# Kernel optimization log

Hardware: AMD Instinct MI355X
Metric: run time of the kernel (lower is better)

Reference implementation:

```python
import jax, jax.numpy as jnp
import numpy as np

NUM_HEADS = 12
HEAD_DIM = 64  # d_out // num_heads = 768 // 12


def setup_inputs() -> dict:
    key = jax.random.key(0)
    k1, k2 = jax.random.split(key)
    x = jax.random.normal(k1, (2, 2048, 768), dtype=jnp.float32)
    # torch Linear weight: [d_out, d_in], y = x @ W.T
    Wq = jax.random.normal(k2, (768, 768), dtype=jnp.float32) * 0.02
    return {"x": x, "Wq": Wq}


def reference(x, Wq):
    b, n, d_in = x.shape
    H, hd = NUM_HEADS, HEAD_DIM
    d_out = H * hd
    # NOTE: the original module uses Wq for queries, keys AND values.
    qkv = x @ Wq.T                                   # [b, n, d_out]
    h = qkv.reshape(b, n, H, hd).transpose(0, 2, 1, 3)  # [b, H, n, hd]
    scores = jnp.einsum('bhqd,bhkd->bhqk', h, h)      # [b, H, n, n]
    causal = jnp.triu(jnp.ones((n, n), dtype=bool), k=1)
    scores = jnp.where(causal, -jnp.inf, scores)
    attn = jax.nn.softmax(scores / jnp.sqrt(jnp.float32(hd)), axis=-1)
    ctx = jnp.einsum('bhqk,bhkd->bhqd', attn, h)      # [b, H, n, hd]
    # faithful to source: transpose(-2,-1) -> [b, H, hd, n], then view(b, n, d_out)
    ctx = ctx.transpose(0, 1, 3, 2)
    return ctx.reshape(b, n, d_out)
```

## Files before the change

kernel.cpp:

```cpp
#include <hip/hip_runtime.h>
#include <math.h>

typedef __attribute__((ext_vector_type(8))) short  short8;
typedef __attribute__((ext_vector_type(4))) float  floatx4;

#define MFMA16(a, b, c) __builtin_amdgcn_mfma_f32_16x16x32_bf16(a, b, c, 0, 0, 0)

constexpr int NSEQ = 2048;
constexpr int DIN  = 768;
constexpr int NH   = 12;
constexpr size_t NX = (size_t)2 * NSEQ * DIN;
constexpr size_t NW = (size_t)DIN * DIN;
constexpr float QSCALE = 0.18033688011112042f;

__device__ __forceinline__ ushort f2bf(float f) {
    unsigned u = __float_as_uint(f);
    u += 0x7FFF + ((u >> 16) & 1);
    return (ushort)(u >> 16);
}
__device__ __forceinline__ float bf2f(ushort u) {
    return __uint_as_float(((unsigned)u) << 16);
}
__device__ __forceinline__ unsigned cvt_pk_bf16(float lo, float hi) {
    unsigned r;
    asm("v_cvt_pk_bf16_f32 %0, %1, %2" : "=v"(r) : "v"(lo), "v"(hi));
    return r;
}

__global__ __launch_bounds__(256)
void cvt_bf16(const float* __restrict__ x, const float* __restrict__ Wq,
              ushort* __restrict__ dst)
{
    size_t i = ((size_t)blockIdx.x * 256 + threadIdx.x) * 8;
    const float* s = (i < NX) ? (x + i) : (Wq + (i - NX));
    float4 f0 = ((const float4*)s)[0];
    float4 f1 = ((const float4*)s)[1];
    short8 o;
    o[0] = (short)f2bf(f0.x); o[1] = (short)f2bf(f0.y);
    o[2] = (short)f2bf(f0.z); o[3] = (short)f2bf(f0.w);
    o[4] = (short)f2bf(f1.x); o[5] = (short)f2bf(f1.y);
    o[6] = (short)f2bf(f1.z); o[7] = (short)f2bf(f1.w);
    *(short8*)(dst + i) = o;
}

__global__ __launch_bounds__(256, 3)
void qkv_mfma(const ushort* __restrict__ xb, const ushort* __restrict__ wb,
              ushort* __restrict__ h)
{
    __shared__ ushort As[64 * 72];
    __shared__ ushort Bs[64 * 72];

    const int tid  = threadIdx.x;
    const int w    = tid >> 6;
    const int lane = tid & 63;
    const int m    = lane & 15;
    const int quad = lane >> 4;
    const int r0   = blockIdx.x * 64;
    const int c0   = blockIdx.y * 64;
    const int mrow0 = (w & 1) * 32;
    const int ncol0 = (w >> 1) * 32;

    floatx4 C[2][2] = {};
    short8 ar[2], br[2];

    #pragma unroll
    for (int i = 0; i < 2; ++i) {
        int id = tid + i * 256;
        ar[i] = *(const short8*)(xb + (size_t)(r0 + (id >> 3)) * DIN + (id & 7) * 8);
        br[i] = *(const short8*)(wb + (size_t)(c0 + (id >> 3)) * DIN + (id & 7) * 8);
    }

    for (int kk = 0; kk < 12; ++kk) {
        __syncthreads();
        #pragma unroll
        for (int i = 0; i < 2; ++i) {
            int id = tid + i * 256;
            *(short8*)&As[(id >> 3) * 72 + (id & 7) * 8] = ar[i];
            *(short8*)&Bs[(id >> 3) * 72 + (id & 7) * 8] = br[i];
        }
        if (kk < 11) {
            const int k0 = (kk + 1) * 64;
            #pragma unroll
            for (int i = 0; i < 2; ++i) {
                int id = tid + i * 256;
                ar[i] = *(const short8*)(xb + (size_t)(r0 + (id >> 3)) * DIN + k0 + (id & 7) * 8);
                br[i] = *(const short8*)(wb + (size_t)(c0 + (id >> 3)) * DIN + k0 + (id & 7) * 8);
            }
        }
        __syncthreads();

        #pragma unroll
        for (int kt2 = 0; kt2 < 2; ++kt2) {
            short8 a0 = *(const short8*)&As[(mrow0 + m)      * 72 + kt2 * 32 + quad * 8];
            short8 a1 = *(const short8*)&As[(mrow0 + 16 + m) * 72 + kt2 * 32 + quad * 8];
            short8 b0 = *(const short8*)&Bs[(ncol0 + m)      * 72 + kt2 * 32 + quad * 8];
            short8 b1 = *(const short8*)&Bs[(ncol0 + 16 + m) * 72 + kt2 * 32 + quad * 8];
            C[0][0] = MFMA16(a0, b0, C[0][0]);
            C[0][1] = MFMA16(a0, b1, C[0][1]);
            C[1][0] = MFMA16(a1, b0, C[1][0]);
            C[1][1] = MFMA16(a1, b1, C[1][1]);
        }
    }

    #pragma unroll
    for (int mt = 0; mt < 2; ++mt)
        #pragma unroll
        for (int nt = 0; nt < 2; ++nt) {
            int cg = c0 + ncol0 + nt * 16 + m;
            int head = cg >> 6, d = cg & 63;
            #pragma unroll
            for (int r = 0; r < 4; ++r) {
                int rg = r0 + mrow0 + mt * 16 + quad * 4 + r;
                int b = rg >> 11, q = rg & 2047;
                h[((size_t)(b * NH + head) * NSEQ + q) * 64 + d] = f2bf(C[mt][nt][r]);
            }
        }
}

__global__ __launch_bounds__(128, 3)
void attn_mfma(const ushort* __restrict__ h, float* __restrict__ out)
{
    __shared__ ushort Ks[64 * 72];
    __shared__ ushort Vt[64 * 72];
    __shared__ ushort Ps[2 * 16 * 72];

    const int tid  = threadIdx.x;
    const int w    = tid >> 6;
    const int lane = tid & 63;
    const int m    = lane & 15;
    const int quad = lane >> 4;

    const int xi = blockIdx.x;
    const int bh = blockIdx.y;
    const int t  = bh >> 2;
    const int qt = (t & 1) ? xi : (63 - xi);
    const int q0 = qt * 32;
    const int wq = q0 + w * 16;
    const int nkt = (qt >> 1) + 1;
    const ushort* __restrict__ Hh = h + (size_t)bh * NSEQ * 64;

    short8 qa[2];
    #pragma unroll
    for (int kt2 = 0; kt2 < 2; ++kt2) {
        short8 raw = *(const short8*)(Hh + (size_t)(wq + m) * 64 + kt2 * 32 + quad * 8);
        #pragma unroll
        for (int j = 0; j < 8; ++j)
            qa[kt2][j] = (short)f2bf(bf2f((ushort)raw[j]) * QSCALE);
    }

    floatx4 O[4] = {};
    float lacc = 0.0f;
    ushort* Psw = Ps + w * 16 * 72;

    const int kr2  = (tid & 31) * 2;
    const int part = tid >> 5;
    const int db   = part * 16;

    short8 pre[4];
    {
        const ushort* src = Hh + (size_t)kr2 * 64 + db;
        pre[0] = *(const short8*)src;
        pre[1] = *(const short8*)(src + 8);
        pre[2] = *(const short8*)(src + 64);
        pre[3] = *(const short8*)(src + 72);
    }

    for (int kt = 0; kt < nkt; ++kt) {
        __syncthreads();
        *(short8*)&Ks[kr2       * 72 + db]     = pre[0];
        *(short8*)&Ks[kr2       * 72 + db + 8] = pre[1];
        *(short8*)&Ks[(kr2 + 1) * 72 + db]     = pre[2];
        *(short8*)&Ks[(kr2 + 1) * 72 + db + 8] = pre[3];
        union { short8 v; ushort u[8]; } a0, a1, b0, b1;
        a0.v = pre[0]; a1.v = pre[1]; b0.v = pre[2]; b1.v = pre[3];
        #pragma unroll
        for (int i = 0; i < 8; ++i) {
            *(unsigned*)&Vt[(db + i)     * 72 + kr2] = (unsigned)a0.u[i] | ((unsigned)b0.u[i] << 16);
            *(unsigned*)&Vt[(db + 8 + i) * 72 + kr2] = (unsigned)a1.u[i] | ((unsigned)b1.u[i] << 16);
        }
        if (kt + 1 < nkt) {
            const ushort* src = Hh + (size_t)((kt + 1) * 64 + kr2) * 64 + db;
            pre[0] = *(const short8*)src;
            pre[1] = *(const short8*)(src + 8);
            pre[2] = *(const short8*)(src + 64);
            pre[3] = *(const short8*)(src + 72);
        }
        __syncthreads();

        floatx4 S[4] = {};
        #pragma unroll
        for (int kt2 = 0; kt2 < 2; ++kt2)
            #pragma unroll
            for (int mt = 0; mt < 4; ++mt) {
                short8 ka = *(const short8*)&Ks[(mt * 16 + m) * 72 + kt2 * 32 + quad * 8];
                S[mt] = MFMA16(ka, qa[kt2], S[mt]);
            }

        const int lim = wq + m - kt * 64;
        if (kt == nkt - 1) {
            #pragma unroll
            for (int mt = 0; mt < 4; ++mt) {
                float p0 = (mt * 16 + quad * 4 + 0 <= lim) ? exp2f(S[mt][0]) : 0.0f;
                float p1 = (mt * 16 + quad * 4 + 1 <= lim) ? exp2f(S[mt][1]) : 0.0f;
                float p2 = (mt * 16 + quad * 4 + 2 <= lim) ? exp2f(S[mt][2]) : 0.0f;
                float p3 = (mt * 16 + quad * 4 + 3 <= lim) ? exp2f(S[mt][3]) : 0.0f;
                lacc += (p0 + p1) + (p2 + p3);
                uint2 pw;
                pw.x = cvt_pk_bf16(p0, p1);
                pw.y = cvt_pk_bf16(p2, p3);
                *(uint2*)&Psw[m * 72 + mt * 16 + quad * 4] = pw;
            }
        } else {
            #pragma unroll
            for (int mt = 0; mt < 4; ++mt) {
                float p0 = exp2f(S[mt][0]);
                float p1 = exp2f(S[mt][1]);
                float p2 = exp2f(S[mt][2]);
                float p3 = exp2f(S[mt][3]);
                lacc += (p0 + p1) + (p2 + p3);
                uint2 pw;
                pw.x = cvt_pk_bf16(p0, p1);
                pw.y = cvt_pk_bf16(p2, p3);
                *(uint2*)&Psw[m * 72 + mt * 16 + quad * 4] = pw;
            }
        }

        #pragma unroll
        for (int kt2 = 0; kt2 < 2; ++kt2) {
            short8 pb = *(const short8*)&Psw[m * 72 + kt2 * 32 + quad * 8];
            #pragma unroll
            for (int mt = 0; mt < 4; ++mt) {
                short8 va = *(const short8*)&Vt[(mt * 16 + m) * 72 + kt2 * 32 + quad * 8];
                O[mt] = MFMA16(va, pb, O[mt]);
            }
        }
    }

    lacc += __shfl_xor(lacc, 16);
    lacc += __shfl_xor(lacc, 32);
    float linv = 1.0f / lacc;

    #pragma unroll
    for (int mt = 0; mt < 4; ++mt)
        #pragma unroll
        for (int r = 0; r < 4; ++r) {
            int d = mt * 16 + quad * 4 + r;
            out[((size_t)bh * 64 + d) * NSEQ + q0 + w * 16 + m] = O[mt][r] * linv;
        }
}

extern "C" void kernel_launch(void* const* d_in, const int* in_sizes, int n_in,
                              void* d_out, int out_size, void* d_ws, size_t ws_size,
                              hipStream_t stream)
{
    (void)in_sizes; (void)n_in; (void)out_size; (void)ws_size;
    const float* x  = (const float*)d_in[0];
    const float* Wq = (const float*)d_in[1];
    float* out = (float*)d_out;

    ushort* xb = (ushort*)d_ws;
    ushort* wb = xb + NX;
    ushort* hb = wb + NW;

    cvt_bf16<<<dim3((NX + NW) / (8 * 256)), dim3(256), 0, stream>>>(x, Wq, xb);
    qkv_mfma<<<dim3(64, 12), dim3(256), 0, stream>>>(xb, wb, hb);
    attn_mfma<<<dim3(64, 24), dim3(128), 0, stream>>>(hb, out);
}
```

Measured before the change: 119.4 us.

## Split attention key range across waves with per-wave LDS and final reduction

The attention kernel now gives each of the two waves in a block all 32 queries, and the waves take alternating 32-key tiles, each with its own K, V-transpose and P buffers. This removes the block-wide barriers from the key loop and trims causal waste by using a 32-key granularity. Partial O and row sums are combined through shared memory at the end. The QKV GEMM also swaps __syncthreads for an lgkmcnt wait plus s_barrier. The trade-offs are more accumulator registers, a reduction epilogue, and load imbalance between waves when the number of key tiles is odd.

```diff
diff --git a/kernel.cpp b/kernel.cpp
--- a/kernel.cpp
+++ b/kernel.cpp
@@ -25,6 +25,10 @@
     unsigned r;
     asm("v_cvt_pk_bf16_f32 %0, %1, %2" : "=v"(r) : "v"(lo), "v"(hi));
     return r;
+}
+__device__ __forceinline__ void bar_lds() {
+    asm volatile("s_waitcnt lgkmcnt(0)" ::: "memory");
+    __builtin_amdgcn_s_barrier();
 }
 
 __global__ __launch_bounds__(256)
@@ -71,7 +75,7 @@
     }
 
     for (int kk = 0; kk < 12; ++kk) {
-        __syncthreads();
+        bar_lds();
         #pragma unroll
         for (int i = 0; i < 2; ++i) {
             int id = tid + i * 256;
@@ -87,7 +91,7 @@
                 br[i] = *(const short8*)(wb + (size_t)(c0 + (id >> 3)) * DIN + k0 + (id & 7) * 8);
             }
         }
-        __syncthreads();
+        bar_lds();
 
         #pragma unroll
         for (int kt2 = 0; kt2 < 2; ++kt2) {
@@ -120,9 +124,7 @@
 __global__ __launch_bounds__(128, 3)
 void attn_mfma(const ushort* __restrict__ h, float* __restrict__ out)
 {
-    __shared__ ushort Ks[64 * 72];
-    __shared__ ushort Vt[64 * 72];
-    __shared__ ushort Ps[2 * 16 * 72];
+    __shared__ ushort sm[10752];
 
     const int tid  = threadIdx.x;
     const int w    = tid >> 6;
@@ -132,120 +134,142 @@
 
     const int xi = blockIdx.x;
     const int bh = blockIdx.y;
-    const int t  = bh >> 2;
-    const int qt = (t & 1) ? xi : (63 - xi);
+    const int qt = ((bh >> 2) & 1) ? xi : (63 - xi);
     const int q0 = qt * 32;
-    const int wq = q0 + w * 16;
-    const int nkt = (qt >> 1) + 1;
+    const int nkt = qt + 1;
     const ushort* __restrict__ Hh = h + (size_t)bh * NSEQ * 64;
 
-    short8 qa[2];
-    #pragma unroll
-    for (int kt2 = 0; kt2 < 2; ++kt2) {
-        short8 raw = *(const short8*)(Hh + (size_t)(wq + m) * 64 + kt2 * 32 + quad * 8);
-        #pragma unroll
-        for (int j = 0; j < 8; ++j)
-            qa[kt2][j] = (short)f2bf(bf2f((ushort)raw[j]) * QSCALE);
-    }
-
-    floatx4 O[4] = {};
-    float lacc = 0.0f;
-    ushort* Psw = Ps + w * 16 * 72;
-
-    const int kr2  = (tid & 31) * 2;
-    const int part = tid >> 5;
-    const int db   = part * 16;
+    ushort* Ks = sm + w * 5376;
+    ushort* Vt = Ks + 32 * 66;
+    ushort* Ps = Vt + 64 * 34;
+
+    short8 qa[2][2];
+    #pragma unroll
+    for (int s = 0; s < 2; ++s)
+        #pragma unroll
+        for (int kt2 = 0; kt2 < 2; ++kt2) {
+            short8 raw = *(const short8*)(Hh + (size_t)(q0 + s * 16 + m) * 64 + kt2 * 32 + quad * 8);
+            #pragma unroll
+            for (int j = 0; j < 8; ++j)
+                qa[s][kt2][j] = (short)f2bf(bf2f((ushort)raw[j]) * QSCALE);
+        }
+
+    floatx4 O[4][2] = {};
+    float lacc[2] = {0.0f, 0.0f};
+
+    const int kr2 = (lane & 15) * 2;
+    const int db  = quad * 16;
 
     short8 pre[4];
     {
-        const ushort* src = Hh + (size_t)kr2 * 64 + db;
+        const ushort* src = Hh + (size_t)(w * 32 + kr2) * 64 + db;
         pre[0] = *(const short8*)src;
         pre[1] = *(const short8*)(src + 8);
         pre[2] = *(const short8*)(src + 64);
         pre[3] = *(const short8*)(src + 72);
     }
 
-    for (int kt = 0; kt < nkt; ++kt) {
-        __syncthreads();
-        *(short8*)&Ks[kr2       * 72 + db]     = pre[0];
-        *(short8*)&Ks[kr2       * 72 + db + 8] = pre[1];
-        *(short8*)&Ks[(kr2 + 1) * 72 + db]     = pre[2];
-        *(short8*)&Ks[(kr2 + 1) * 72 + db + 8] = pre[3];
+    for (int kt = w; kt < nkt; kt += 2) {
+        *(short8*)&Ks[kr2       * 66 + db]     = pre[0];
+        *(short8*)&Ks[kr2       * 66 + db + 8] = pre[1];
+        *(short8*)&Ks[(kr2 + 1) * 66 + db]     = pre[2];
+        *(short8*)&Ks[(kr2 + 1) * 66 + db + 8] = pre[3];
         union { short8 v; ushort u[8]; } a0, a1, b0, b1;
         a0.v = pre[0]; a1.v = pre[1]; b0.v = pre[2]; b1.v = pre[3];
         #pragma unroll
         for (int i = 0; i < 8; ++i) {
-            *(unsigned*)&Vt[(db + i)     * 72 + kr2] = (unsigned)a0.u[i] | ((unsigned)b0.u[i] << 16);
-            *(unsigned*)&Vt[(db + 8 + i) * 72 + kr2] = (unsigned)a1.u[i] | ((unsigned)b1.u[i] << 16);
-        }
-        if (kt + 1 < nkt) {
-            const ushort* src = Hh + (size_t)((kt + 1) * 64 + kr2) * 64 + db;
+            *(unsigned*)&Vt[(db + i)     * 34 + kr2] = (unsigned)a0.u[i] | ((unsigned)b0.u[i] << 16);
+            *(unsigned*)&Vt[(db + 8 + i) * 34 + kr2] = (unsigned)a1.u[i] | ((unsigned)b1.u[i] << 16);
+        }
+        if (kt + 2 < nkt) {
+            const ushort* src = Hh + (size_t)((kt + 2) * 32 + kr2) * 64 + db;
             pre[0] = *(const short8*)src;
             pre[1] = *(const short8*)(src + 8);
             pre[2] = *(const short8*)(src + 64);
             pre[3] = *(const short8*)(src + 72);
         }
-        __syncthreads();
-
-        floatx4 S[4] = {};
+
+        floatx4 S[2][2] = {};
         #pragma unroll
         for (int kt2 = 0; kt2 < 2; ++kt2)
             #pragma unroll
-            for (int mt = 0; mt < 4; ++mt) {
-                short8 ka = *(const short8*)&Ks[(mt * 16 + m) * 72 + kt2 * 32 + quad * 8];
-                S[mt] = MFMA16(ka, qa[kt2], S[mt]);
-            }
-
-        const int lim = wq + m - kt * 64;
-        if (kt == nkt - 1) {
-            #pragma unroll
-            for (int mt = 0; mt < 4; ++mt) {
-                float p0 = (mt * 16 + quad * 4 + 0 <= lim) ? exp2f(S[mt][0]) : 0.0f;
-                float p1 = (mt * 16 + quad * 4 + 1 <= lim) ? exp2f(S[mt][1]) : 0.0f;
-                float p2 = (mt * 16 + quad * 4 + 2 <= lim) ? exp2f(S[mt][2]) : 0.0f;
-                float p3 = (mt * 16 + quad * 4 + 3 <= lim) ? exp2f(S[mt][3]) : 0.0f;
-                lacc += (p0 + p1) + (p2 + p3);
+            for (int mt = 0; mt < 2; ++mt) {
+                short8 ka = *(const short8*)&Ks[(mt * 16 + m) * 66 + kt2 * 32 + quad * 8];
+                S[mt][0] = MFMA16(ka, qa[0][kt2], S[mt][0]);
+                S[mt][1] = MFMA16(ka, qa[1][kt2], S[mt][1]);
+            }
+
+        const bool diag = (kt == qt);
+        #pragma unroll
+        for (int s = 0; s < 2; ++s) {
+            const int lim = s * 16 + m;
+            #pragma unroll
+            for (int mt = 0; mt < 2; ++mt) {
+                const int kb = mt * 16 + quad * 4;
+                float p0, p1, p2, p3;
+                if (diag) {
+                    p0 = (kb + 0 <= lim) ? exp2f(S[mt][s][0]) : 0.0f;
+                    p1 = (kb + 1 <= lim) ? exp2f(S[mt][s][1]) : 0.0f;
+                    p2 = (kb + 2 <= lim) ? exp2f(S[mt][s][2]) : 0.0f;
+                    p3 = (kb + 3 <= lim) ? exp2f(S[mt][s][3]) : 0.0f;
+                } else {
+                    p0 = exp2f(S[mt][s][0]);
+                    p1 = exp2f(S[mt][s][1]);
+                    p2 = exp2f(S[mt][s][2]);
+                    p3 = exp2f(S[mt][s][3]);
+                }
+                lacc[s] += (p0 + p1) + (p2 + p3);
                 uint2 pw;
                 pw.x = cvt_pk_bf16(p0, p1);
                 pw.y = cvt_pk_bf16(p2, p3);
-                *(uint2*)&Psw[m * 72 + mt * 16 + quad * 4] = pw;
-            }
-        } else {
-            #pragma unroll
-            for (int mt = 0; mt < 4; ++mt) {
-                float p0 = exp2f(S[mt][0]);
-                float p1 = exp2f(S[mt][1]);
-                float p2 = exp2f(S[mt][2]);
-                float p3 = exp2f(S[mt][3]);
-                lacc += (p0 + p1) + (p2 + p3);
-                uint2 pw;
-                pw.x = cvt_pk_bf16(p0, p1);
-                pw.y = cvt_pk_bf16(p2, p3);
-                *(uint2*)&Psw[m * 72 + mt * 16 + quad * 4] = pw;
-            }
-        }
-
-        #pragma unroll
-        for (int kt2 = 0; kt2 < 2; ++kt2) {
-            short8 pb = *(const short8*)&Psw[m * 72 + kt2 * 32 + quad * 8];
-            #pragma unroll
-            for (int mt = 0; mt < 4; ++mt) {
-                short8 va = *(const short8*)&Vt[(mt * 16 + m) * 72 + kt2 * 32 + quad * 8];
-                O[mt] = MFMA16(va, pb, O[mt]);
-            }
-        }
-    }
-
-    lacc += __shfl_xor(lacc, 16);
-    lacc += __shfl_xor(lacc, 32);
-    float linv = 1.0f / lacc;
-
+                *(uint2*)&Ps[s * 544 + m * 34 + kb] = pw;
+            }
+        }
+
+        short8 pb0 = *(const short8*)&Ps[0 * 544 + m * 34 + quad * 8];
+        short8 pb1 = *(const short8*)&Ps[1 * 544 + m * 34 + quad * 8];
+        #pragma unroll
+        for (int mt = 0; mt < 4; ++mt) {
+            short8 va = *(const short8*)&Vt[(mt * 16 + m) * 34 + quad * 8];
+            O[mt][0] = MFMA16(va, pb0, O[mt][0]);
+            O[mt][1] = MFMA16(va, pb1, O[mt][1]);
+        }
+    }
+
+    #pragma unroll
+    for (int s = 0; s < 2; ++s) {
+        lacc[s] += __shfl_xor(lacc[s], 16);
+        lacc[s] += __shfl_xor(lacc[s], 32);
+    }
+
+    __syncthreads();
+    float* OM = (float*)sm;
+    float* LM = (float*)sm + 2 * 64 * 33;
+    #pragma unroll
+    for (int mt = 0; mt < 4; ++mt)
+        #pragma unroll
+        for (int s = 0; s < 2; ++s)
+            #pragma unroll
+            for (int r = 0; r < 4; ++r) {
+                int d = mt * 16 + quad * 4 + r;
+                OM[((size_t)w * 64 + d) * 33 + s * 16 + m] = O[mt][s][r];
+            }
+    if (quad == 0) {
+        LM[w * 32 + 0 * 16 + m] = lacc[0];
+        LM[w * 32 + 1 * 16 + m] = lacc[1];
+    }
+    __syncthreads();
+
+    const int ow = 1 - w;
+    float lf = lacc[w] + LM[ow * 32 + w * 16 + m];
+    float linv = 1.0f / lf;
     #pragma unroll
     for (int mt = 0; mt < 4; ++mt)
         #pragma unroll
         for (int r = 0; r < 4; ++r) {
             int d = mt * 16 + quad * 4 + r;
-            out[((size_t)bh * 64 + d) * NSEQ + q0 + w * 16 + m] = O[mt][r] * linv;
+            float v = O[mt][w][r] + OM[((size_t)ow * 64 + d) * 33 + w * 16 + m];
+            out[((size_t)bh * 64 + d) * NSEQ + q0 + w * 16 + m] = v * linv;
         }
 }
 
```

Result: slower. 189.4 us (+58.6%).
